# Optimization experiments

Measured on AMD Instinct MI355X. Metric: run time of the kernel, lower is better.

## Reference

```python
import jax, jax.numpy as jnp
import numpy as np

B, T, D, H, O = 16384, 64, 64, 256, 1


def setup_inputs() -> dict:
    key = jax.random.key(0)
    ks = jax.random.split(key, 16)
    s = 0.05
    inp = {
        "x": jax.random.normal(ks[0], (B, T, D), dtype=jnp.float32),
        # RNNCell layer1: h1 = tanh(x @ W_ih1.T + b_ih1 + h1 @ W_hh1.T + b_hh1)
        "W_ih1": jax.random.normal(ks[1], (H, D), dtype=jnp.float32) * s,
        "b_ih1": jax.random.normal(ks[2], (H,), dtype=jnp.float32) * s,
        "W_hh1": jax.random.normal(ks[3], (H, H), dtype=jnp.float32) * s,
        "b_hh1": jax.random.normal(ks[4], (H,), dtype=jnp.float32) * s,
        # RNNCell layer2 (input is h1, size H)
        "W_ih2": jax.random.normal(ks[5], (H, H), dtype=jnp.float32) * s,
        "b_ih2": jax.random.normal(ks[6], (H,), dtype=jnp.float32) * s,
        "W_hh2": jax.random.normal(ks[7], (H, H), dtype=jnp.float32) * s,
        "b_hh2": jax.random.normal(ks[8], (H,), dtype=jnp.float32) * s,
        # output heads
        "W_o1": jax.random.normal(ks[9], (O, H), dtype=jnp.float32) * s,
        "b_o1": jax.random.normal(ks[10], (O,), dtype=jnp.float32) * s,
        "W_o2": jax.random.normal(ks[11], (O, H), dtype=jnp.float32) * s,
        "b_o2": jax.random.normal(ks[12], (O,), dtype=jnp.float32) * s,
        # gate: Linear(2H, H)
        "W_g": jax.random.normal(ks[13], (H, 2 * H), dtype=jnp.float32) * s,
        "b_g": jax.random.normal(ks[14], (H,), dtype=jnp.float32) * s,
    }
    return inp


def _gated_rnn(x, W_ih1, b_ih1, W_hh1, b_hh1, W_ih2, b_ih2, W_hh2, b_hh2,
               W_o1, b_o1, W_o2, b_o2, W_g, b_g):
    b = x.shape[0]
    h1_0 = jnp.zeros((b, H), dtype=x.dtype)
    h2_0 = jnp.zeros((b, H), dtype=x.dtype)
    u_0 = jnp.ones((b, H), dtype=x.dtype)

    # Precompute input projections for all timesteps: [T, B, H]
    x_proj = jnp.einsum('btd,hd->tbh', x, W_ih1) + b_ih1

    def step(carry, xp_t):
        h1, h2, u = carry
        h1 = jnp.tanh(xp_t + h1 @ W_hh1.T + b_hh1)
        z2 = jnp.tanh(h1 @ W_ih2.T + b_ih2 + h2 @ W_hh2.T + b_hh2)
        h2 = u * z2 + (1.0 - u) * h2
        out = jnp.tanh(h1 @ W_o1.T + b_o1) + jnp.tanh(h2 @ W_o2.T + b_o2)
        u = jax.nn.sigmoid(jnp.concatenate([h1, h2], axis=1) @ W_g.T + b_g)
        return (h1, h2, u), out

    _, outs = jax.lax.scan(step, (h1_0, h2_0, u_0), x_proj)  # outs: [T, B, O]
    outs = jnp.transpose(outs, (1, 0, 2))  # [B, T, O]
    if outs.shape[2] == 1:
        outs = outs[:, :, 0]  # mirror .squeeze(2)
    return outs


def reference(x, W_ih1, b_ih1, W_hh1, b_hh1, W_ih2, b_ih2, W_hh2, b_hh2,
              W_o1, b_o1, W_o2, b_o2, W_g, b_g):
    return _gated_rnn(x, W_ih1, b_ih1, W_hh1, b_hh1, W_ih2, b_ih2, W_hh2,
                      b_hh2, W_o1, b_o1, W_o2, b_o2, W_g, b_g)
```

## Files before the change

### kernel.cpp

```cpp
#include <hip/hip_runtime.h>
#include <hip/hip_bf16.h>

typedef __bf16 bf16_t;
typedef __bf16 bf16x8 __attribute__((ext_vector_type(8)));
typedef float f32x4 __attribute__((ext_vector_type(4)));

#define HDIM 256
#define TSTEPS 64
#define DIN 64
#define BM 64
#define NBLK 256

__device__ __forceinline__ float fast_tanh(float x) {
    float e = __builtin_amdgcn_exp2f(x * 2.8853900817779268f);
    return 1.0f - 2.0f * __builtin_amdgcn_rcpf(e + 1.0f);
}
__device__ __forceinline__ float fast_sigmoid(float x) {
    float e = __builtin_amdgcn_exp2f(-x * 1.4426950408889634f);
    return __builtin_amdgcn_rcpf(1.0f + e);
}

__device__ __forceinline__ unsigned lds_addr(int row, int kb) {
    return (unsigned)(row * 512 + (kb ^ ((row & 7) << 4)));
}
__device__ __forceinline__ unsigned lx_addr(int row, int kb) {
    return (unsigned)(row * 128 + (kb ^ ((row & 7) << 4)));
}

__global__ void pack_w(const float* __restrict__ s0, const float* __restrict__ s1,
                       int ksplit, int stride0, int stride1, int off0, int off1,
                       int KC, bf16_t* __restrict__ dst) {
    int idx = blockIdx.x * 256 + threadIdx.x;
    int total = 256 * KC * 32;
    if (idx >= total) return;
    int i = idx & 7;
    int lane = (idx >> 3) & 63;
    int chunk = idx >> 9;
    int n2 = chunk & 1;
    int rest = chunk >> 1;
    int kc = rest % KC, wv = rest / KC;
    int nt = wv * 2 + n2;
    int n = nt * 16 + (lane & 15);
    int k = kc * 32 + ((lane >> 4) * 8) + i;
    float v = (k < ksplit) ? s0[n * stride0 + off0 + k]
                           : s1[n * stride1 + off1 + (k - ksplit)];
    dst[idx] = (bf16_t)v;
}

__global__ void pack_bias(const float* __restrict__ b_ih1, const float* __restrict__ b_hh1,
                          const float* __restrict__ b_ih2, const float* __restrict__ b_hh2,
                          const float* __restrict__ b_g,
                          float* __restrict__ bias1, float* __restrict__ bias2a,
                          float* __restrict__ biasg) {
    int j = threadIdx.x;
    bias1[j] = b_ih1[j] + b_hh1[j];
    bias2a[j] = b_ih2[j] + b_hh2[j];
    biasg[j] = b_g[j];
}

#define ISSUE(BUF, PB, N)                                            \
    _Pragma("unroll") for (int c = 0; c < (N); ++c)                  \
        BUF[c] = *(const bf16x8*)((PB) + c * 512 + (lane << 3));

#define GEMM_PH(NKK, BUF, ASRC, KC0, ACC)                                             \
    _Pragma("unroll") for (int kk = 0; kk < (NKK); ++kk) {                            \
        bf16x8 a_[4];                                                                 \
        _Pragma("unroll") for (int mt = 0; mt < 4; ++mt)                              \
            a_[mt] = *(const bf16x8*)((ASRC) + lds_addr(mt * 16 + l15,                \
                                                        ((KC0) + kk) * 64 + l4 * 16));\
        _Pragma("unroll") for (int mt = 0; mt < 4; ++mt) {                            \
            ACC[mt][0] = __builtin_amdgcn_mfma_f32_16x16x32_bf16(a_[mt], BUF[kk * 2 + 0], ACC[mt][0], 0, 0, 0); \
            ACC[mt][1] = __builtin_amdgcn_mfma_f32_16x16x32_bf16(a_[mt], BUF[kk * 2 + 1], ACC[mt][1], 0, 0, 0); \
        }                                                                             \
    }

__global__ __launch_bounds__(512, 2) void rnn_main(
    const float* __restrict__ x,
    const bf16_t* __restrict__ pw_ih1,
    const bf16_t* __restrict__ pw_hh1,
    const bf16_t* __restrict__ pw_2a,
    const bf16_t* __restrict__ pw_2b,
    const bf16_t* __restrict__ pw_3,
    const float* __restrict__ bias1v, const float* __restrict__ bias2av,
    const float* __restrict__ biasgv,
    const float* __restrict__ wo1, const float* __restrict__ bo1p,
    const float* __restrict__ wo2, const float* __restrict__ bo2p,
    float* __restrict__ out) {
    __shared__ char lds[73728];
    char* lh1 = lds;
    char* lh2 = lds + 32768;
    char* lx  = lds + 65536;

    const int tid = threadIdx.x;
    const int wave = tid >> 6, lane = tid & 63;
    const int l15 = lane & 15, l4 = lane >> 4;
    const int b0 = blockIdx.x * BM;

    {
        int4 z = {0, 0, 0, 0};
        for (int i = tid; i < 4096; i += 512) ((int4*)lds)[i] = z;
    }

    f32x4 u_reg[4][2], h2_reg[4][2];
#pragma unroll
    for (int mt = 0; mt < 4; ++mt)
#pragma unroll
        for (int n2 = 0; n2 < 2; ++n2) {
            u_reg[mt][n2] = (f32x4){1.f, 1.f, 1.f, 1.f};
            h2_reg[mt][n2] = (f32x4){0.f, 0.f, 0.f, 0.f};
        }

    float bias1_r[2], bias2a_r[2], biasg_r[2];
#pragma unroll
    for (int n2 = 0; n2 < 2; ++n2) {
        int col = wave * 32 + n2 * 16 + l15;
        bias1_r[n2] = bias1v[col];
        bias2a_r[n2] = bias2av[col];
        biasg_r[n2] = biasgv[col];
    }
    const float bo1 = bo1p[0], bo2 = bo2p[0];
    const int orow = tid >> 3, oseg = tid & 7;
    const int xrow = tid >> 3, xc16 = (tid & 7) * 16;
    const float* xbase = x + (size_t)(b0 + xrow) * (TSTEPS * DIN) + (tid & 7) * 8;

    const bf16_t* base_ih1 = pw_ih1 + wave * 2048;
    const bf16_t* base_hh1 = pw_hh1 + wave * 8192;
    const bf16_t* base_2a  = pw_2a  + wave * 16384;
    const bf16_t* base_2b  = pw_2b  + wave * 8192;
    const bf16_t* base_3   = pw_3   + wave * 8192;

    bf16x8 bufA[8], bufB[8];

    ISSUE(bufA, base_ih1, 4);
    {
        f32x4 xv0 = __builtin_nontemporal_load((const f32x4*)xbase);
        f32x4 xv1 = __builtin_nontemporal_load((const f32x4*)(xbase + 4));
        bf16x8 xa;
        xa[0] = (bf16_t)xv0[0]; xa[1] = (bf16_t)xv0[1]; xa[2] = (bf16_t)xv0[2]; xa[3] = (bf16_t)xv0[3];
        xa[4] = (bf16_t)xv1[0]; xa[5] = (bf16_t)xv1[1]; xa[6] = (bf16_t)xv1[2]; xa[7] = (bf16_t)xv1[3];
        *(bf16x8*)(lx + lx_addr(xrow, xc16)) = xa;
    }

    __syncthreads();

    for (int t = 0; t < TSTEPS; ++t) {
        f32x4 acc[4][2];
#pragma unroll
        for (int mt = 0; mt < 4; ++mt)
#pragma unroll
            for (int n2 = 0; n2 < 2; ++n2) acc[mt][n2] = (f32x4){0.f, 0.f, 0.f, 0.f};
        ISSUE(bufB, base_hh1, 8);
        f32x4 xv0, xv1;
        {
            int tn = t + 1; if (tn > TSTEPS - 1) tn = TSTEPS - 1;
            const float* xp = xbase + tn * DIN;
            xv0 = __builtin_nontemporal_load((const f32x4*)xp);
            xv1 = __builtin_nontemporal_load((const f32x4*)(xp + 4));
        }
#pragma unroll
        for (int kk = 0; kk < 2; ++kk) {
            bf16x8 a_[4];
#pragma unroll
            for (int mt = 0; mt < 4; ++mt)
                a_[mt] = *(const bf16x8*)(lx + lx_addr(mt * 16 + l15, kk * 64 + l4 * 16));
#pragma unroll
            for (int mt = 0; mt < 4; ++mt) {
                acc[mt][0] = __builtin_amdgcn_mfma_f32_16x16x32_bf16(a_[mt], bufA[kk * 2 + 0], acc[mt][0], 0, 0, 0);
                acc[mt][1] = __builtin_amdgcn_mfma_f32_16x16x32_bf16(a_[mt], bufA[kk * 2 + 1], acc[mt][1], 0, 0, 0);
            }
        }
        ISSUE(bufA, base_hh1 + 4096, 8);
        GEMM_PH(4, bufB, lh1, 0, acc)
        ISSUE(bufB, base_2a, 8);
        GEMM_PH(4, bufA, lh1, 4, acc)

        float h1n[4][2][4];
#pragma unroll
        for (int mt = 0; mt < 4; ++mt)
#pragma unroll
            for (int n2 = 0; n2 < 2; ++n2)
#pragma unroll
                for (int r = 0; r < 4; ++r)
                    h1n[mt][n2][r] = fast_tanh(acc[mt][n2][r] + bias1_r[n2]);
        __syncthreads();
#pragma unroll
        for (int mt = 0; mt < 4; ++mt)
#pragma unroll
            for (int n2 = 0; n2 < 2; ++n2)
#pragma unroll
                for (int r = 0; r < 4; ++r)
                    *(bf16_t*)(lh1 + lds_addr(mt * 16 + l4 * 4 + r,
                                              (wave * 32 + n2 * 16 + l15) * 2)) = (bf16_t)h1n[mt][n2][r];
        __syncthreads();

        f32x4 accz[4][2];
#pragma unroll
        for (int mt = 0; mt < 4; ++mt)
#pragma unroll
            for (int n2 = 0; n2 < 2; ++n2) accz[mt][n2] = (f32x4){0.f, 0.f, 0.f, 0.f};
        ISSUE(bufA, base_2a + 4096, 8);
        GEMM_PH(4, bufB, lh1, 0, accz)
        ISSUE(bufB, base_2a + 8192, 8);
        GEMM_PH(4, bufA, lh1, 4, accz)
        ISSUE(bufA, base_2a + 12288, 8);
        GEMM_PH(4, bufB, lh2, 0, accz)
        ISSUE(bufB, base_2b, 8);
        GEMM_PH(4, bufA, lh2, 4, accz)

#pragma unroll
        for (int mt = 0; mt < 4; ++mt)
#pragma unroll
            for (int n2 = 0; n2 < 2; ++n2)
#pragma unroll
                for (int r = 0; r < 4; ++r) {
                    float z2 = fast_tanh(accz[mt][n2][r] + bias2a_r[n2]);
                    float un = u_reg[mt][n2][r];
                    h2_reg[mt][n2][r] = un * z2 + (1.f - un) * h2_reg[mt][n2][r];
                }
        __syncthreads();
#pragma unroll
        for (int mt = 0; mt < 4; ++mt)
#pragma unroll
            for (int n2 = 0; n2 < 2; ++n2)
#pragma unroll
                for (int r = 0; r < 4; ++r)
                    *(bf16_t*)(lh2 + lds_addr(mt * 16 + l4 * 4 + r,
                                              (wave * 32 + n2 * 16 + l15) * 2)) = (bf16_t)h2_reg[mt][n2][r];
        {
            bf16x8 xa;
            xa[0] = (bf16_t)xv0[0]; xa[1] = (bf16_t)xv0[1]; xa[2] = (bf16_t)xv0[2]; xa[3] = (bf16_t)xv0[3];
            xa[4] = (bf16_t)xv1[0]; xa[5] = (bf16_t)xv1[1]; xa[6] = (bf16_t)xv1[2]; xa[7] = (bf16_t)xv1[3];
            *(bf16x8*)(lx + lx_addr(xrow, xc16)) = xa;
        }

        f32x4 accg[4][2];
#pragma unroll
        for (int mt = 0; mt < 4; ++mt)
#pragma unroll
            for (int n2 = 0; n2 < 2; ++n2) accg[mt][n2] = (f32x4){0.f, 0.f, 0.f, 0.f};
        ISSUE(bufA, base_2b + 4096, 8);
        GEMM_PH(4, bufB, lh1, 0, accg)
        __syncthreads();

        ISSUE(bufB, base_3, 8);
        GEMM_PH(4, bufA, lh1, 4, accg)
        ISSUE(bufA, base_3 + 4096, 4);
        GEMM_PH(4, bufB, lh2, 0, accg)
        ISSUE(bufB, base_3 + 6144, 4);
        GEMM_PH(2, bufA, lh2, 4, accg)
        ISSUE(bufA, base_ih1, 4);
        GEMM_PH(2, bufB, lh2, 6, accg)

#pragma unroll
        for (int mt = 0; mt < 4; ++mt)
#pragma unroll
            for (int n2 = 0; n2 < 2; ++n2)
#pragma unroll
                for (int r = 0; r < 4; ++r)
                    u_reg[mt][n2][r] = fast_sigmoid(accg[mt][n2][r] + biasg_r[n2]);

        float s1 = 0.f, s2 = 0.f;
#pragma unroll
        for (int c = 0; c < 4; ++c) {
            int kb = oseg * 64 + c * 16;
            bf16x8 hv1 = *(const bf16x8*)(lh1 + lds_addr(orow, kb));
            bf16x8 hv2 = *(const bf16x8*)(lh2 + lds_addr(orow, kb));
            const float* w1p = wo1 + oseg * 32 + c * 8;
            const float* w2p = wo2 + oseg * 32 + c * 8;
            float4 w10 = *(const float4*)w1p, w11 = *(const float4*)(w1p + 4);
            float4 w20 = *(const float4*)w2p, w21 = *(const float4*)(w2p + 4);
            s1 += (float)hv1[0] * w10.x + (float)hv1[1] * w10.y + (float)hv1[2] * w10.z + (float)hv1[3] * w10.w;
            s1 += (float)hv1[4] * w11.x + (float)hv1[5] * w11.y + (float)hv1[6] * w11.z + (float)hv1[7] * w11.w;
            s2 += (float)hv2[0] * w20.x + (float)hv2[1] * w20.y + (float)hv2[2] * w20.z + (float)hv2[3] * w20.w;
            s2 += (float)hv2[4] * w21.x + (float)hv2[5] * w21.y + (float)hv2[6] * w21.z + (float)hv2[7] * w21.w;
        }
        s1 += __shfl_xor(s1, 1, 8); s1 += __shfl_xor(s1, 2, 8); s1 += __shfl_xor(s1, 4, 8);
        s2 += __shfl_xor(s2, 1, 8); s2 += __shfl_xor(s2, 2, 8); s2 += __shfl_xor(s2, 4, 8);
        if (oseg == 0)
            out[(size_t)(b0 + orow) * TSTEPS + t] = fast_tanh(s1 + bo1) + fast_tanh(s2 + bo2);
    }
}

extern "C" void kernel_launch(void* const* d_in, const int* in_sizes, int n_in,
                              void* d_out, int out_size, void* d_ws, size_t ws_size,
                              hipStream_t stream) {
    const float* x = (const float*)d_in[0];
    const float* W_ih1 = (const float*)d_in[1];
    const float* b_ih1 = (const float*)d_in[2];
    const float* W_hh1 = (const float*)d_in[3];
    const float* b_hh1 = (const float*)d_in[4];
    const float* W_ih2 = (const float*)d_in[5];
    const float* b_ih2 = (const float*)d_in[6];
    const float* W_hh2 = (const float*)d_in[7];
    const float* b_hh2 = (const float*)d_in[8];
    const float* W_o1 = (const float*)d_in[9];
    const float* b_o1 = (const float*)d_in[10];
    const float* W_o2 = (const float*)d_in[11];
    const float* b_o2 = (const float*)d_in[12];
    const float* W_g = (const float*)d_in[13];
    const float* b_g = (const float*)d_in[14];

    char* ws = (char*)d_ws;
    bf16_t* pw_ih1 = (bf16_t*)(ws + 0);
    bf16_t* pw_hh1 = (bf16_t*)(ws + 32768);
    bf16_t* pw_2a = (bf16_t*)(ws + 163840);
    bf16_t* pw_2b = (bf16_t*)(ws + 425984);
    bf16_t* pw_3 = (bf16_t*)(ws + 557056);
    float* bias1 = (float*)(ws + 688128);
    float* bias2a = (float*)(ws + 689152);
    float* biasg = (float*)(ws + 690176);

    pack_w<<<32 * 2, 256, 0, stream>>>(W_ih1, W_ih1, 64, 64, 64, 0, 0, 2, pw_ih1);
    pack_w<<<32 * 8, 256, 0, stream>>>(W_hh1, W_hh1, 256, 256, 256, 0, 0, 8, pw_hh1);
    pack_w<<<32 * 16, 256, 0, stream>>>(W_ih2, W_hh2, 256, 256, 256, 0, 0, 16, pw_2a);
    pack_w<<<32 * 8, 256, 0, stream>>>(W_g, W_g, 256, 512, 512, 0, 0, 8, pw_2b);
    pack_w<<<32 * 8, 256, 0, stream>>>(W_g, W_g, 256, 512, 512, 256, 0, 8, pw_3);
    pack_bias<<<1, 256, 0, stream>>>(b_ih1, b_hh1, b_ih2, b_hh2, b_g, bias1, bias2a, biasg);

    rnn_main<<<NBLK, 512, 0, stream>>>(x, pw_ih1, pw_hh1, pw_2a, pw_2b, pw_3,
                                       bias1, bias2a, biasg, W_o1, b_o1, W_o2, b_o2,
                                       (float*)d_out);
}
```

Before: 2.328 ms.

## Triple-buffer weight registers, keep h2 in LDS, stage outputs for coalesced store

Replaces the two-buffer weight prefetch with three register buffers (R0/R1/R2), so each weight chunk is issued two GEMM phases ahead of its use. h2 is no longer held in registers; it is read back from LDS, which frees VGPRs for the extra buffer. Launch bounds drop to one block per CU so the larger register and LDS footprint fits. Per-step outputs are collected in LDS and written with vectorized stores at the end, and barriers become custom s_barrier calls with volatile LDS accesses. The cost is half the occupancy and extra LDS reads, with the volatile accesses possibly limiting compiler scheduling.

```diff
diff --git a/kernel.cpp b/kernel.cpp
--- a/kernel.cpp
+++ b/kernel.cpp
@@ -4,6 +4,7 @@
 typedef __bf16 bf16_t;
 typedef __bf16 bf16x8 __attribute__((ext_vector_type(8)));
 typedef float f32x4 __attribute__((ext_vector_type(4)));
+typedef int i32x4 __attribute__((ext_vector_type(4)));
 
 #define HDIM 256
 #define TSTEPS 64
@@ -26,6 +27,21 @@
 __device__ __forceinline__ unsigned lx_addr(int row, int kb) {
     return (unsigned)(row * 128 + (kb ^ ((row & 7) << 4)));
 }
+
+__device__ __forceinline__ bf16x8 lds_ld8(const char* p) {
+    return *(const volatile bf16x8*)p;
+}
+__device__ __forceinline__ void lds_st1(char* p, bf16_t v) {
+    *(volatile bf16_t*)p = v;
+}
+
+#define BAR()                                      \
+    do {                                           \
+        __builtin_amdgcn_sched_barrier(0);         \
+        asm volatile("s_waitcnt lgkmcnt(0)");      \
+        __builtin_amdgcn_s_barrier();              \
+        __builtin_amdgcn_sched_barrier(0);         \
+    } while (0)
 
 __global__ void pack_w(const float* __restrict__ s0, const float* __restrict__ s1,
                        int ksplit, int stride0, int stride1, int off0, int off1,
@@ -66,15 +82,15 @@
     _Pragma("unroll") for (int kk = 0; kk < (NKK); ++kk) {                            \
         bf16x8 a_[4];                                                                 \
         _Pragma("unroll") for (int mt = 0; mt < 4; ++mt)                              \
-            a_[mt] = *(const bf16x8*)((ASRC) + lds_addr(mt * 16 + l15,                \
-                                                        ((KC0) + kk) * 64 + l4 * 16));\
+            a_[mt] = lds_ld8((ASRC) + lds_addr(mt * 16 + l15,                         \
+                                               ((KC0) + kk) * 64 + l4 * 16));         \
         _Pragma("unroll") for (int mt = 0; mt < 4; ++mt) {                            \
             ACC[mt][0] = __builtin_amdgcn_mfma_f32_16x16x32_bf16(a_[mt], BUF[kk * 2 + 0], ACC[mt][0], 0, 0, 0); \
             ACC[mt][1] = __builtin_amdgcn_mfma_f32_16x16x32_bf16(a_[mt], BUF[kk * 2 + 1], ACC[mt][1], 0, 0, 0); \
         }                                                                             \
     }
 
-__global__ __launch_bounds__(512, 2) void rnn_main(
+__global__ __launch_bounds__(512, 1) void rnn_main(
     const float* __restrict__ x,
     const bf16_t* __restrict__ pw_ih1,
     const bf16_t* __restrict__ pw_hh1,
@@ -86,10 +102,11 @@
     const float* __restrict__ wo1, const float* __restrict__ bo1p,
     const float* __restrict__ wo2, const float* __restrict__ bo2p,
     float* __restrict__ out) {
-    __shared__ char lds[73728];
+    __shared__ char lds[90112];
     char* lh1 = lds;
     char* lh2 = lds + 32768;
     char* lx  = lds + 65536;
+    volatile float* lout = (volatile float*)(lds + 73728);
 
     const int tid = threadIdx.x;
     const int wave = tid >> 6, lane = tid & 63;
@@ -97,18 +114,15 @@
     const int b0 = blockIdx.x * BM;
 
     {
-        int4 z = {0, 0, 0, 0};
-        for (int i = tid; i < 4096; i += 512) ((int4*)lds)[i] = z;
-    }
-
-    f32x4 u_reg[4][2], h2_reg[4][2];
+        i32x4 z = {0, 0, 0, 0};
+        for (int i = tid; i < 4096; i += 512) ((volatile i32x4*)lds)[i] = z;
+    }
+
+    f32x4 u_reg[4][2];
 #pragma unroll
     for (int mt = 0; mt < 4; ++mt)
 #pragma unroll
-        for (int n2 = 0; n2 < 2; ++n2) {
-            u_reg[mt][n2] = (f32x4){1.f, 1.f, 1.f, 1.f};
-            h2_reg[mt][n2] = (f32x4){0.f, 0.f, 0.f, 0.f};
-        }
+        for (int n2 = 0; n2 < 2; ++n2) u_reg[mt][n2] = (f32x4){1.f, 1.f, 1.f, 1.f};
 
     float bias1_r[2], bias2a_r[2], biasg_r[2];
 #pragma unroll
@@ -129,19 +143,20 @@
     const bf16_t* base_2b  = pw_2b  + wave * 8192;
     const bf16_t* base_3   = pw_3   + wave * 8192;
 
-    bf16x8 bufA[8], bufB[8];
-
-    ISSUE(bufA, base_ih1, 4);
+    bf16x8 R0[8], R1[8], R2[8];
+
     {
         f32x4 xv0 = __builtin_nontemporal_load((const f32x4*)xbase);
         f32x4 xv1 = __builtin_nontemporal_load((const f32x4*)(xbase + 4));
         bf16x8 xa;
         xa[0] = (bf16_t)xv0[0]; xa[1] = (bf16_t)xv0[1]; xa[2] = (bf16_t)xv0[2]; xa[3] = (bf16_t)xv0[3];
         xa[4] = (bf16_t)xv1[0]; xa[5] = (bf16_t)xv1[1]; xa[6] = (bf16_t)xv1[2]; xa[7] = (bf16_t)xv1[3];
-        *(bf16x8*)(lx + lx_addr(xrow, xc16)) = xa;
-    }
-
-    __syncthreads();
+        *(volatile bf16x8*)(lx + lx_addr(xrow, xc16)) = xa;
+    }
+    ISSUE(R0, base_ih1, 4);
+    ISSUE(R1, base_hh1, 8);
+    ISSUE(R2, base_hh1 + 4096, 8);
+    BAR();
 
     for (int t = 0; t < TSTEPS; ++t) {
         f32x4 acc[4][2];
@@ -149,7 +164,19 @@
         for (int mt = 0; mt < 4; ++mt)
 #pragma unroll
             for (int n2 = 0; n2 < 2; ++n2) acc[mt][n2] = (f32x4){0.f, 0.f, 0.f, 0.f};
-        ISSUE(bufB, base_hh1, 8);
+#pragma unroll
+        for (int kk = 0; kk < 2; ++kk) {
+            bf16x8 a_[4];
+#pragma unroll
+            for (int mt = 0; mt < 4; ++mt)
+                a_[mt] = lds_ld8(lx + lx_addr(mt * 16 + l15, kk * 64 + l4 * 16));
+#pragma unroll
+            for (int mt = 0; mt < 4; ++mt) {
+                acc[mt][0] = __builtin_amdgcn_mfma_f32_16x16x32_bf16(a_[mt], R0[kk * 2 + 0], acc[mt][0], 0, 0, 0);
+                acc[mt][1] = __builtin_amdgcn_mfma_f32_16x16x32_bf16(a_[mt], R0[kk * 2 + 1], acc[mt][1], 0, 0, 0);
+            }
+        }
+        ISSUE(R0, base_2a, 8);
         f32x4 xv0, xv1;
         {
             int tn = t + 1; if (tn > TSTEPS - 1) tn = TSTEPS - 1;
@@ -157,22 +184,10 @@
             xv0 = __builtin_nontemporal_load((const f32x4*)xp);
             xv1 = __builtin_nontemporal_load((const f32x4*)(xp + 4));
         }
-#pragma unroll
-        for (int kk = 0; kk < 2; ++kk) {
-            bf16x8 a_[4];
-#pragma unroll
-            for (int mt = 0; mt < 4; ++mt)
-                a_[mt] = *(const bf16x8*)(lx + lx_addr(mt * 16 + l15, kk * 64 + l4 * 16));
-#pragma unroll
-            for (int mt = 0; mt < 4; ++mt) {
-                acc[mt][0] = __builtin_amdgcn_mfma_f32_16x16x32_bf16(a_[mt], bufA[kk * 2 + 0], acc[mt][0], 0, 0, 0);
-                acc[mt][1] = __builtin_amdgcn_mfma_f32_16x16x32_bf16(a_[mt], bufA[kk * 2 + 1], acc[mt][1], 0, 0, 0);
-            }
-        }
-        ISSUE(bufA, base_hh1 + 4096, 8);
-        GEMM_PH(4, bufB, lh1, 0, acc)
-        ISSUE(bufB, base_2a, 8);
-        GEMM_PH(4, bufA, lh1, 4, acc)
+        GEMM_PH(4, R1, lh1, 0, acc)
+        ISSUE(R1, base_2a + 4096, 8);
+        GEMM_PH(4, R2, lh1, 4, acc)
+        ISSUE(R2, base_2a + 8192, 8);
 
         float h1n[4][2][4];
 #pragma unroll
@@ -182,31 +197,32 @@
 #pragma unroll
                 for (int r = 0; r < 4; ++r)
                     h1n[mt][n2][r] = fast_tanh(acc[mt][n2][r] + bias1_r[n2]);
-        __syncthreads();
+        BAR();
 #pragma unroll
         for (int mt = 0; mt < 4; ++mt)
 #pragma unroll
             for (int n2 = 0; n2 < 2; ++n2)
 #pragma unroll
                 for (int r = 0; r < 4; ++r)
-                    *(bf16_t*)(lh1 + lds_addr(mt * 16 + l4 * 4 + r,
-                                              (wave * 32 + n2 * 16 + l15) * 2)) = (bf16_t)h1n[mt][n2][r];
-        __syncthreads();
+                    lds_st1(lh1 + lds_addr(mt * 16 + l4 * 4 + r,
+                                           (wave * 32 + n2 * 16 + l15) * 2), (bf16_t)h1n[mt][n2][r]);
+        BAR();
 
         f32x4 accz[4][2];
 #pragma unroll
         for (int mt = 0; mt < 4; ++mt)
 #pragma unroll
             for (int n2 = 0; n2 < 2; ++n2) accz[mt][n2] = (f32x4){0.f, 0.f, 0.f, 0.f};
-        ISSUE(bufA, base_2a + 4096, 8);
-        GEMM_PH(4, bufB, lh1, 0, accz)
-        ISSUE(bufB, base_2a + 8192, 8);
-        GEMM_PH(4, bufA, lh1, 4, accz)
-        ISSUE(bufA, base_2a + 12288, 8);
-        GEMM_PH(4, bufB, lh2, 0, accz)
-        ISSUE(bufB, base_2b, 8);
-        GEMM_PH(4, bufA, lh2, 4, accz)
-
+        GEMM_PH(4, R0, lh1, 0, accz)
+        ISSUE(R0, base_2a + 12288, 8);
+        GEMM_PH(4, R1, lh1, 4, accz)
+        ISSUE(R1, base_2b, 8);
+        GEMM_PH(4, R2, lh2, 0, accz)
+        ISSUE(R2, base_2b + 4096, 8);
+        GEMM_PH(4, R0, lh2, 4, accz)
+        ISSUE(R0, base_3, 8);
+
+        float h2n[4][2][4];
 #pragma unroll
         for (int mt = 0; mt < 4; ++mt)
 #pragma unroll
@@ -214,23 +230,25 @@
 #pragma unroll
                 for (int r = 0; r < 4; ++r) {
                     float z2 = fast_tanh(accz[mt][n2][r] + bias2a_r[n2]);
+                    float h2o = (float)*(const volatile bf16_t*)(lh2 + lds_addr(mt * 16 + l4 * 4 + r,
+                                                                                (wave * 32 + n2 * 16 + l15) * 2));
                     float un = u_reg[mt][n2][r];
-                    h2_reg[mt][n2][r] = un * z2 + (1.f - un) * h2_reg[mt][n2][r];
+                    h2n[mt][n2][r] = un * z2 + (1.f - un) * h2o;
                 }
-        __syncthreads();
+        BAR();
 #pragma unroll
         for (int mt = 0; mt < 4; ++mt)
 #pragma unroll
             for (int n2 = 0; n2 < 2; ++n2)
 #pragma unroll
                 for (int r = 0; r < 4; ++r)
-                    *(bf16_t*)(lh2 + lds_addr(mt * 16 + l4 * 4 + r,
-                                              (wave * 32 + n2 * 16 + l15) * 2)) = (bf16_t)h2_reg[mt][n2][r];
+                    lds_st1(lh2 + lds_addr(mt * 16 + l4 * 4 + r,
+                                           (wave * 32 + n2 * 16 + l15) * 2), (bf16_t)h2n[mt][n2][r]);
         {
             bf16x8 xa;
             xa[0] = (bf16_t)xv0[0]; xa[1] = (bf16_t)xv0[1]; xa[2] = (bf16_t)xv0[2]; xa[3] = (bf16_t)xv0[3];
             xa[4] = (bf16_t)xv1[0]; xa[5] = (bf16_t)xv1[1]; xa[6] = (bf16_t)xv1[2]; xa[7] = (bf16_t)xv1[3];
-            *(bf16x8*)(lx + lx_addr(xrow, xc16)) = xa;
+            *(volatile bf16x8*)(lx + lx_addr(xrow, xc16)) = xa;
         }
 
         f32x4 accg[4][2];
@@ -238,18 +256,18 @@
         for (int mt = 0; mt < 4; ++mt)
 #pragma unroll
             for (int n2 = 0; n2 < 2; ++n2) accg[mt][n2] = (f32x4){0.f, 0.f, 0.f, 0.f};
-        ISSUE(bufA, base_2b + 4096, 8);
-        GEMM_PH(4, bufB, lh1, 0, accg)
-        __syncthreads();
-
-        ISSUE(bufB, base_3, 8);
-        GEMM_PH(4, bufA, lh1, 4, accg)
-        ISSUE(bufA, base_3 + 4096, 4);
-        GEMM_PH(4, bufB, lh2, 0, accg)
-        ISSUE(bufB, base_3 + 6144, 4);
-        GEMM_PH(2, bufA, lh2, 4, accg)
-        ISSUE(bufA, base_ih1, 4);
-        GEMM_PH(2, bufB, lh2, 6, accg)
+        GEMM_PH(4, R1, lh1, 0, accg)
+        ISSUE(R1, base_3 + 4096, 4);
+        BAR();
+
+        GEMM_PH(4, R2, lh1, 4, accg)
+        ISSUE(R2, base_3 + 6144, 4);
+        GEMM_PH(4, R0, lh2, 0, accg)
+        ISSUE(R0, base_ih1, 4);
+        GEMM_PH(2, R1, lh2, 4, accg)
+        ISSUE(R1, base_hh1, 8);
+        GEMM_PH(2, R2, lh2, 6, accg)
+        ISSUE(R2, base_hh1 + 4096, 8);
 
 #pragma unroll
         for (int mt = 0; mt < 4; ++mt)
@@ -263,8 +281,8 @@
 #pragma unroll
         for (int c = 0; c < 4; ++c) {
             int kb = oseg * 64 + c * 16;
-            bf16x8 hv1 = *(const bf16x8*)(lh1 + lds_addr(orow, kb));
-            bf16x8 hv2 = *(const bf16x8*)(lh2 + lds_addr(orow, kb));
+            bf16x8 hv1 = lds_ld8(lh1 + lds_addr(orow, kb));
+            bf16x8 hv2 = lds_ld8(lh2 + lds_addr(orow, kb));
             const float* w1p = wo1 + oseg * 32 + c * 8;
             const float* w2p = wo2 + oseg * 32 + c * 8;
             float4 w10 = *(const float4*)w1p, w11 = *(const float4*)(w1p + 4);
@@ -277,7 +295,19 @@
         s1 += __shfl_xor(s1, 1, 8); s1 += __shfl_xor(s1, 2, 8); s1 += __shfl_xor(s1, 4, 8);
         s2 += __shfl_xor(s2, 1, 8); s2 += __shfl_xor(s2, 2, 8); s2 += __shfl_xor(s2, 4, 8);
         if (oseg == 0)
-            out[(size_t)(b0 + orow) * TSTEPS + t] = fast_tanh(s1 + bo1) + fast_tanh(s2 + bo2);
+            lout[orow * TSTEPS + t] = fast_tanh(s1 + bo1) + fast_tanh(s2 + bo2);
+    }
+
+    BAR();
+    {
+        float o[8];
+#pragma unroll
+        for (int i = 0; i < 8; ++i) o[i] = lout[tid * 8 + i];
+        float* op = out + (size_t)b0 * TSTEPS + tid * 8;
+        f32x4 o0 = {o[0], o[1], o[2], o[3]};
+        f32x4 o1 = {o[4], o[5], o[6], o[7]};
+        *(f32x4*)op = o0;
+        *(f32x4*)(op + 4) = o1;
     }
 }
 
```

New measurement: 7.232 ms. +210.7%, slower.
